# Kernel tuning notes

Measured on AMD Instinct MI355X. Metric: run time of the kernel, lower is better.

The kernel has to match this reference:

```python
import jax, jax.numpy as jnp
import numpy as np

W_INTRA = 1.0
W_INTER = 1.0
W_REG = 1.0
LOSS_WEIGHT = 1.0


def setup_inputs() -> dict:
    key = jax.random.key(0)
    k1, k2, k3 = jax.random.split(key, 3)
    N, C, H, W, K = 2, 80, 512, 512, 32
    pred_emb = jax.random.normal(k1, (N, C, H, W), dtype=jnp.float32)
    gt_objmask = jax.random.randint(k2, (N, K, H, W), 0, 2).astype(jnp.bool_)
    gt_classes = jax.random.randint(k3, (N, K), 0, C)
    return {"pred_emb": pred_emb, "gt_objmask": gt_objmask, "gt_classes": gt_classes}


def _emb_loss_single(pred_emb, mask, classes):
    # pred_emb: (C,H,W) float, mask: (K,H,W) bool, classes: (K,) int
    emb = pred_emb[classes]                      # (K,H,W) gather by class id
    m = mask.astype(pred_emb.dtype)
    cnt = m.sum(axis=(1, 2))                     # (K,) masked pixel counts
    s = (emb * m).sum(axis=(1, 2))               # masked sum
    s2 = (emb * emb * m).sum(axis=(1, 2))        # masked sum of squares
    valid = cnt > 0
    safe = jnp.where(valid, cnt, 1.0)
    mean = jnp.where(valid, s / safe, 0.0)       # torch: mean of masked_select (0 if empty)
    var = jnp.where(valid, s2 / safe - mean * mean, 0.0)  # biased variance (unbiased=False)
    K = classes.shape[0]
    # pairwise inter-instance term over same-class pairs j<k
    diff2 = (mean[:, None] - mean[None, :]) ** 2
    same = classes[:, None] == classes[None, :]
    triu = jnp.triu(jnp.ones((K, K), dtype=bool), k=1)
    inter = jnp.sum(jnp.where(same & triu, jnp.maximum(1.0 - diff2, 0.0), 0.0))
    reg = jnp.mean(mean ** 2)
    intra = jnp.mean(var)
    return W_INTER * inter + W_REG * reg + W_INTRA * intra


def reference(pred_emb, gt_objmask, gt_classes):
    per_image = jax.vmap(_emb_loss_single)(pred_emb, gt_objmask, gt_classes)  # (N,)
    return per_image.mean() * LOSS_WEIGHT * 0.1
```

## Files before the change

kernel.cpp:

```cpp
#include <hip/hip_runtime.h>

#define N_IMG 2
#define K_OBJ 32
#define C_CH  80
#define HW    (512 * 512)
#define NK    (N_IMG * K_OBJ)

#define BPN 32
#define BT  256
#define SPAN (BPN * BT)
#define NV16 (HW / 16)
#define ITERS (NV16 / SPAN)


__global__ __launch_bounds__(BT) void partial_kernel(
    const float* __restrict__ pred,
    const unsigned char* __restrict__ mask,
    const int* __restrict__ classes,
    float* __restrict__ ws)
{
    const int nk  = blockIdx.x / BPN;
    const int blk = blockIdx.x % BPN;
    const int n   = nk / K_OBJ;
    const int c   = classes[nk];

    const float4* __restrict__ embv =
        (const float4*)(pred + (size_t)(n * C_CH + c) * HW);
    const uint4* __restrict__ mv =
        (const uint4*)(mask + (size_t)nk * HW);

    unsigned int cnt_i = 0;
    float s = 0.0f, s2 = 0.0f;

    const int base = blk * BT + threadIdx.x;

#define ACCB(w, b, e) do {                                   \
        float v_ = (((w) >> (8*(b))) & 1u) ? (e) : 0.0f;     \
        s += v_; s2 = fmaf(v_, (e), s2);                     \
    } while (0)

    #pragma unroll
    for (int it = 0; it < ITERS; ++it) {
        const int i = base + it * SPAN;
        const uint4  m  = mv[i];
        const float4 e0 = embv[4*i + 0];
        const float4 e1 = embv[4*i + 1];
        const float4 e2 = embv[4*i + 2];
        const float4 e3 = embv[4*i + 3];

        unsigned int t = m.x + m.y + m.z + m.w;
        cnt_i += (t * 0x01010101u) >> 24;

        ACCB(m.x,0,e0.x); ACCB(m.x,1,e0.y); ACCB(m.x,2,e0.z); ACCB(m.x,3,e0.w);
        ACCB(m.y,0,e1.x); ACCB(m.y,1,e1.y); ACCB(m.y,2,e1.z); ACCB(m.y,3,e1.w);
        ACCB(m.z,0,e2.x); ACCB(m.z,1,e2.y); ACCB(m.z,2,e2.z); ACCB(m.z,3,e2.w);
        ACCB(m.w,0,e3.x); ACCB(m.w,1,e3.y); ACCB(m.w,2,e3.z); ACCB(m.w,3,e3.w);
    }
#undef ACCB

    float cnt = (float)cnt_i;
    #pragma unroll
    for (int off = 32; off > 0; off >>= 1) {
        cnt += __shfl_down(cnt, off);
        s   += __shfl_down(s,   off);
        s2  += __shfl_down(s2,  off);
    }

    __shared__ float sm[3][BT / 64];
    const int lane = threadIdx.x & 63;
    const int wv   = threadIdx.x >> 6;
    if (lane == 0) { sm[0][wv] = cnt; sm[1][wv] = s; sm[2][wv] = s2; }
    __syncthreads();
    if (threadIdx.x == 0) {
        float tc = 0.f, ts = 0.f, t2 = 0.f;
        #pragma unroll
        for (int w = 0; w < BT / 64; ++w) {
            tc += sm[0][w]; ts += sm[1][w]; t2 += sm[2][w];
        }
        float* dst = ws + (size_t)blk * 3 * NK;
        dst[0 * NK + nk] = tc;
        dst[1 * NK + nk] = ts;
        dst[2 * NK + nk] = t2;
    }
}

__global__ __launch_bounds__(256) void finalize(
    const float* __restrict__ ws,
    const int* __restrict__ classes,
    float* __restrict__ out)
{
    const int t  = threadIdx.x;
    const int nk = t & 63;
    const int g  = t >> 6;

    float cnt = 0.f, s = 0.f, s2 = 0.f;
    #pragma unroll
    for (int b = 0; b < BPN / 4; ++b) {
        const float* src = ws + (size_t)(g * (BPN / 4) + b) * 3 * NK;
        cnt += src[0 * NK + nk];
        s   += src[1 * NK + nk];
        s2  += src[2 * NK + nk];
    }

    __shared__ float pc[4][NK], ps[4][NK], p2[4][NK];
    pc[g][nk] = cnt; ps[g][nk] = s; p2[g][nk] = s2;
    __syncthreads();

    __shared__ float smean[NK];
    __shared__ int   scls[NK];
    float mean = 0.f, var = 0.f;
    if (t < NK) {
        float fc = pc[0][t] + pc[1][t] + pc[2][t] + pc[3][t];
        float fs = ps[0][t] + ps[1][t] + ps[2][t] + ps[3][t];
        float f2 = p2[0][t] + p2[1][t] + p2[2][t] + p2[3][t];
        const bool valid = fc > 0.0f;
        const float safe = valid ? fc : 1.0f;
        mean = valid ? fs / safe : 0.0f;
        var  = valid ? f2 / safe - mean * mean : 0.0f;
        smean[t] = mean;
        scls[t]  = classes[t];
    }
    __syncthreads();

    if (t < NK) {
        const int j  = t & 31;
        const int nb = t & 32;
        float part = (mean * mean + var) * (1.0f / K_OBJ);
        const int cj = scls[t];
        for (int k = j + 1; k < K_OBJ; ++k) {
            if (scls[nb + k] == cj) {
                float d = mean - smean[nb + k];
                float val = 1.0f - d * d;
                part += (val > 0.0f) ? val : 0.0f;
            }
        }
        #pragma unroll
        for (int off = 32; off > 0; off >>= 1) part += __shfl_down(part, off);
        if (t == 0) out[0] = part * (0.1f / N_IMG);
    }
}

extern "C" void kernel_launch(void* const* d_in, const int* in_sizes, int n_in,
                              void* d_out, int out_size, void* d_ws, size_t ws_size,
                              hipStream_t stream) {
    const float* pred = (const float*)d_in[0];
    const unsigned char* mask = (const unsigned char*)d_in[1];
    const int* classes = (const int*)d_in[2];
    float* out = (float*)d_out;
    float* ws = (float*)d_ws;

    partial_kernel<<<NK * BPN, BT, 0, stream>>>(pred, mask, classes, ws);
    finalize<<<1, 256, 0, stream>>>(ws, classes, out);
}
```

Before: 21.84 us.

## Pair same-class instances so one block reads the embedding channel once

Each block scans the class list to find other instances in its image with the same class id. Blocks at odd positions in each same-class group exit early, and blocks at even positions also accumulate their partner's mask against the embedding values already loaded, writing partials for both instances. This avoids re-reading the embedding plane for duplicate-class instances, and the per-thread loop is reshaped to strided uint mask loads with float4 embedding loads. The gain depends on how often classes repeat, which with random ids is rare. In exchange it adds a class scan per block, extra registers and divergent branches.

```diff
diff --git a/kernel.cpp b/kernel.cpp
--- a/kernel.cpp
+++ b/kernel.cpp
@@ -9,8 +9,7 @@
 #define BPN 32
 #define BT  256
 #define SPAN (BPN * BT)
-#define NV16 (HW / 16)
-#define ITERS (NV16 / SPAN)
+#define ITERS 2
 
 
 __global__ __launch_bounds__(BT) void partial_kernel(
@@ -21,66 +20,123 @@
 {
     const int nk  = blockIdx.x / BPN;
     const int blk = blockIdx.x % BPN;
-    const int n   = nk / K_OBJ;
+    const int n   = nk >> 5;
+    const int k   = nk & 31;
     const int c   = classes[nk];
+
+    int p = 0, partner = -1;
+    #pragma unroll
+    for (int j = 0; j < K_OBJ; ++j) {
+        const int cj = classes[n * K_OBJ + j];
+        if (cj == c) {
+            if (j < k) ++p;
+            else if (j > k && partner < 0) partner = j;
+        }
+    }
+    if (p & 1) return;
+    const bool have2 = (partner >= 0) && !(p & 1);
 
     const float4* __restrict__ embv =
         (const float4*)(pred + (size_t)(n * C_CH + c) * HW);
-    const uint4* __restrict__ mv =
-        (const uint4*)(mask + (size_t)nk * HW);
-
-    unsigned int cnt_i = 0;
-    float s = 0.0f, s2 = 0.0f;
+    const unsigned int* __restrict__ mv0 =
+        (const unsigned int*)(mask + (size_t)nk * HW);
+    const unsigned int* __restrict__ mv1 =
+        (const unsigned int*)(mask + (size_t)(n * K_OBJ + (have2 ? partner : k)) * HW);
+
+    unsigned int msum0 = 0, msum1 = 0;
+    float s0 = 0.f, s20 = 0.f, s1 = 0.f, s21 = 0.f;
 
     const int base = blk * BT + threadIdx.x;
 
-#define ACCB(w, b, e) do {                                   \
-        float v_ = (((w) >> (8*(b))) & 1u) ? (e) : 0.0f;     \
-        s += v_; s2 = fmaf(v_, (e), s2);                     \
+#define ACCB(w, b, ev, S, S2) do {                            \
+        float v_ = (((w) >> (8*(b))) & 1u) ? (ev) : 0.0f;     \
+        S += v_; S2 = fmaf(v_, (ev), S2);                     \
     } while (0)
 
     #pragma unroll
     for (int it = 0; it < ITERS; ++it) {
         const int i = base + it * SPAN;
-        const uint4  m  = mv[i];
-        const float4 e0 = embv[4*i + 0];
-        const float4 e1 = embv[4*i + 1];
-        const float4 e2 = embv[4*i + 2];
-        const float4 e3 = embv[4*i + 3];
-
-        unsigned int t = m.x + m.y + m.z + m.w;
-        cnt_i += (t * 0x01010101u) >> 24;
-
-        ACCB(m.x,0,e0.x); ACCB(m.x,1,e0.y); ACCB(m.x,2,e0.z); ACCB(m.x,3,e0.w);
-        ACCB(m.y,0,e1.x); ACCB(m.y,1,e1.y); ACCB(m.y,2,e1.z); ACCB(m.y,3,e1.w);
-        ACCB(m.z,0,e2.x); ACCB(m.z,1,e2.y); ACCB(m.z,2,e2.z); ACCB(m.z,3,e2.w);
-        ACCB(m.w,0,e3.x); ACCB(m.w,1,e3.y); ACCB(m.w,2,e3.z); ACCB(m.w,3,e3.w);
+        float4 e[4];
+        unsigned int ma[4], mb[4];
+        #pragma unroll
+        for (int q = 0; q < 4; ++q) {
+            const int idx = i + q * SPAN * ITERS;
+            (void)idx;
+        }
+        #pragma unroll
+        for (int q = 0; q < 4; ++q) {
+            const int idx = i + q * (SPAN * 2);
+            e[q]  = embv[idx];
+            ma[q] = mv0[idx];
+        }
+        if (have2) {
+            #pragma unroll
+            for (int q = 0; q < 4; ++q) {
+                const int idx = i + q * (SPAN * 2);
+                mb[q] = mv1[idx];
+            }
+        }
+        #pragma unroll
+        for (int q = 0; q < 4; ++q) {
+            msum0 += ma[q];
+            ACCB(ma[q], 0, e[q].x, s0, s20);
+            ACCB(ma[q], 1, e[q].y, s0, s20);
+            ACCB(ma[q], 2, e[q].z, s0, s20);
+            ACCB(ma[q], 3, e[q].w, s0, s20);
+        }
+        if (have2) {
+            #pragma unroll
+            for (int q = 0; q < 4; ++q) {
+                msum1 += mb[q];
+                ACCB(mb[q], 0, e[q].x, s1, s21);
+                ACCB(mb[q], 1, e[q].y, s1, s21);
+                ACCB(mb[q], 2, e[q].z, s1, s21);
+                ACCB(mb[q], 3, e[q].w, s1, s21);
+            }
+        }
     }
 #undef ACCB
 
-    float cnt = (float)cnt_i;
+    float cnt0 = (float)((msum0 * 0x01010101u) >> 24);
+    float cnt1 = (float)((msum1 * 0x01010101u) >> 24);
+
     #pragma unroll
     for (int off = 32; off > 0; off >>= 1) {
-        cnt += __shfl_down(cnt, off);
-        s   += __shfl_down(s,   off);
-        s2  += __shfl_down(s2,  off);
-    }
-
-    __shared__ float sm[3][BT / 64];
+        cnt0 += __shfl_down(cnt0, off);
+        s0   += __shfl_down(s0,   off);
+        s20  += __shfl_down(s20,  off);
+        cnt1 += __shfl_down(cnt1, off);
+        s1   += __shfl_down(s1,   off);
+        s21  += __shfl_down(s21,  off);
+    }
+
+    __shared__ float sm[6][BT / 64];
     const int lane = threadIdx.x & 63;
     const int wv   = threadIdx.x >> 6;
-    if (lane == 0) { sm[0][wv] = cnt; sm[1][wv] = s; sm[2][wv] = s2; }
+    if (lane == 0) {
+        sm[0][wv] = cnt0; sm[1][wv] = s0; sm[2][wv] = s20;
+        sm[3][wv] = cnt1; sm[4][wv] = s1; sm[5][wv] = s21;
+    }
     __syncthreads();
     if (threadIdx.x == 0) {
-        float tc = 0.f, ts = 0.f, t2 = 0.f;
-        #pragma unroll
-        for (int w = 0; w < BT / 64; ++w) {
-            tc += sm[0][w]; ts += sm[1][w]; t2 += sm[2][w];
+        float acc[6];
+        #pragma unroll
+        for (int comp = 0; comp < 6; ++comp) {
+            float a = 0.f;
+            #pragma unroll
+            for (int w = 0; w < BT / 64; ++w) a += sm[comp][w];
+            acc[comp] = a;
         }
         float* dst = ws + (size_t)blk * 3 * NK;
-        dst[0 * NK + nk] = tc;
-        dst[1 * NK + nk] = ts;
-        dst[2 * NK + nk] = t2;
+        dst[0 * NK + nk] = acc[0];
+        dst[1 * NK + nk] = acc[1];
+        dst[2 * NK + nk] = acc[2];
+        if (have2) {
+            const int pk = n * K_OBJ + partner;
+            dst[0 * NK + pk] = acc[3];
+            dst[1 * NK + pk] = acc[4];
+            dst[2 * NK + pk] = acc[5];
+        }
     }
 }
 
@@ -127,9 +183,9 @@
         const int nb = t & 32;
         float part = (mean * mean + var) * (1.0f / K_OBJ);
         const int cj = scls[t];
-        for (int k = j + 1; k < K_OBJ; ++k) {
-            if (scls[nb + k] == cj) {
-                float d = mean - smean[nb + k];
+        for (int kk = j + 1; kk < K_OBJ; ++kk) {
+            if (scls[nb + kk] == cj) {
+                float d = mean - smean[nb + kk];
                 float val = 1.0f - d * d;
                 part += (val > 0.0f) ? val : 0.0f;
             }
```

Result: slower. 22.95 us (+5.1%).
